# Optimization experiments

Hardware: AMD Instinct MI355X
Metric: run time of the kernel (lower is better)

The kernel has to match this reference:

```python
import jax, jax.numpy as jnp
import numpy as np

F = 32          # conf['num_features']
G = 96          # voxel grid extent
N_VOX = 80000   # occupied input voxels
BN_EPS = 1e-5


def _encode(c):
    c = c.astype(np.int64) + 8
    return (c[:, 0] * 512 + c[:, 1]) * 512 + c[:, 2]


def _offsets(ks, dil):
    r = np.arange(-(ks // 2), ks // 2 + 1) * dil
    return np.stack(np.meshgrid(r, r, r, indexing='ij'), -1).reshape(-1, 3)


def _build_map(in_coords, out_coords, offsets):
    # For each kernel offset k and output voxel j, find input voxel index at
    # out_coords[j] + offsets[k]; sentinel = n_in / n_out when absent.
    n_in, n_out = len(in_coords), len(out_coords)
    keys = _encode(in_coords)
    order = np.argsort(keys).astype(np.int32)
    skeys = keys[order]
    K = len(offsets)
    in_map = np.full((K, n_out), n_in, np.int32)
    out_map = np.full((K, n_out), n_out, np.int32)
    base = np.arange(n_out, dtype=np.int32)
    for k, off in enumerate(offsets):
        q = _encode(out_coords + off)
        pos = np.clip(np.searchsorted(skeys, q), 0, n_in - 1)
        valid = skeys[pos] == q
        in_map[k] = np.where(valid, order[pos], n_in)
        out_map[k] = np.where(valid, base, n_out)
    return jnp.asarray(in_map), jnp.asarray(out_map)


def setup_inputs() -> dict:
    rng = np.random.default_rng(0)
    idx = rng.choice(G ** 3, size=N_VOX, replace=False)
    coords = np.stack(np.unravel_index(idx, (G, G, G)), 1).astype(np.int64)
    c2 = np.unique(coords // 2 * 2, axis=0)   # stride-2 coords (enc1 output)
    c4 = np.unique(coords // 4 * 4, axis=0)   # stride-4 coords (c_out.C)

    m1_in, m1_out = _build_map(coords, c2, _offsets(5, 1))  # k5 s2 conv
    m2_in, m2_out = _build_map(c2, c2, _offsets(3, 2))      # enc1 blocks
    m3_in, m3_out = _build_map(c2, c4, _offsets(3, 2))      # conv2 -> c_out.C
    m4_in, m4_out = _build_map(c4, c4, _offsets(3, 4))      # enc2 blocks

    key = jax.random.key(0)
    ks = jax.random.split(key, 8)
    s = 0.05
    return {
        'x_geo': jax.random.normal(ks[0], (N_VOX, 1), jnp.float32),
        'x_col': jax.random.uniform(ks[1], (N_VOX, 3), jnp.float32),
        'w0': jax.random.normal(ks[2], (125, 4, F), jnp.float32) * s,
        'w_e1': jax.random.normal(ks[3], (2, 2, 27, F, F), jnp.float32) * s,
        'g_e1': jnp.ones((2, 2, F), jnp.float32),
        'b_e1': jnp.zeros((2, 2, F), jnp.float32),
        'w2': jax.random.normal(ks[4], (27, F, 2 * F), jnp.float32) * s,
        'w_e2': jax.random.normal(ks[5], (2, 2, 27, 2 * F, 2 * F), jnp.float32) * s,
        'g_e2': jnp.ones((2, 2, 2 * F), jnp.float32),
        'b_e2': jnp.zeros((2, 2, 2 * F), jnp.float32),
        'm1_in': m1_in, 'm1_out': m1_out,
        'm2_in': m2_in, 'm2_out': m2_out,
        'm3_in': m3_in, 'm3_out': m3_out,
        'm4_in': m4_in, 'm4_out': m4_out,
    }


def sparse_conv(feats, W, in_map, out_map):
    # gather -> GEMM -> scatter per kernel offset (lax.scan over K offsets)
    n_out = out_map.shape[1]
    fpad = jnp.concatenate([feats, jnp.zeros((1, feats.shape[1]), feats.dtype)], 0)
    out0 = jnp.zeros((n_out + 1, W.shape[2]), feats.dtype)
    def step(acc, kmw):
        im, om, w = kmw
        return acc.at[om].add(fpad[im] @ w), None
    out, _ = jax.lax.scan(step, out0, (in_map, out_map, W))
    return out[:n_out]


def batch_norm(x, g, b):
    mu = x.mean(0)
    var = ((x - mu) ** 2).mean(0)
    return (x - mu) * jax.lax.rsqrt(var + BN_EPS) * g + b


def basic_block(x, w, g, b, in_map, out_map):
    # ME BasicBlock: conv-BN-ReLU-conv-BN + residual, ReLU
    y = jax.nn.relu(batch_norm(sparse_conv(x, w[0], in_map, out_map), g[0], b[0]))
    y = batch_norm(sparse_conv(y, w[1], in_map, out_map), g[1], b[1])
    return jax.nn.relu(y + x)


def reference(x_geo, x_col, w0, w_e1, g_e1, b_e1, w2, w_e2, g_e2, b_e2,
              m1_in, m1_out, m2_in, m2_out, m3_in, m3_out, m4_in, m4_out):
    x = jnp.concatenate([x_geo, x_col], axis=1)          # ME.cat -> 4 channels
    x = jax.nn.relu(sparse_conv(x, w0, m1_in, m1_out))   # k5 s2 conv + ReLU
    for i in range(2):                                   # enc1 residual blocks
        x = basic_block(x, w_e1[i], g_e1[i], b_e1[i], m2_in, m2_out)
    x = sparse_conv(x, w2, m3_in, m3_out)                # conv2 onto c_out.C
    for i in range(2):                                   # enc2 residual blocks
        x = basic_block(x, w_e2[i], g_e2[i], b_e2[i], m4_in, m4_out)
    return x
```

## Files before the change

kernel.cpp:

```cpp
#include <hip/hip_runtime.h>
#include <hip/hip_bf16.h>


typedef float f4 __attribute__((ext_vector_type(4)));
typedef short short8 __attribute__((ext_vector_type(8)));
typedef short short4v __attribute__((ext_vector_type(4)));

#define BN_EPS 1e-5f

static inline int ceil_div(int a, int b) { return (a + b - 1) / b; }

static __device__ inline float btof(short s) {
    unsigned u = ((unsigned)(unsigned short)s) << 16;
    float f;
    __builtin_memcpy(&f, &u, 4);
    return f;
}
static __device__ inline short ftob(float f) {
    __hip_bfloat16 h = __float2bfloat16(f);
    short s;
    __builtin_memcpy(&s, &h, 2);
    return s;
}

static __device__ inline void gl_lds16(const void* g, void* l) {
    __builtin_amdgcn_global_load_lds(
        (const __attribute__((address_space(1))) void*)g,
        (__attribute__((address_space(3))) void*)l, 16, 0, 0);
}

template <int N>
static __device__ inline void s_wait_vmcnt() {
    static_assert(N >= 0 && N <= 8, "vmcnt range");
    if constexpr (N == 0) asm volatile("s_waitcnt vmcnt(0)" ::: "memory");
    else if constexpr (N == 1) asm volatile("s_waitcnt vmcnt(1)" ::: "memory");
    else if constexpr (N == 2) asm volatile("s_waitcnt vmcnt(2)" ::: "memory");
    else if constexpr (N == 3) asm volatile("s_waitcnt vmcnt(3)" ::: "memory");
    else if constexpr (N == 4) asm volatile("s_waitcnt vmcnt(4)" ::: "memory");
    else if constexpr (N == 5) asm volatile("s_waitcnt vmcnt(5)" ::: "memory");
    else if constexpr (N == 6) asm volatile("s_waitcnt vmcnt(6)" ::: "memory");
    else if constexpr (N == 7) asm volatile("s_waitcnt vmcnt(7)" ::: "memory");
    else asm volatile("s_waitcnt vmcnt(8)" ::: "memory");
}

struct Seg {
    const float* W;
    long long begin, end;
    int K, CIN, COUT;
};

struct ProArgs {
    Seg s[10];
    const float* geo;
    const float* col;
    __hip_bfloat16* x0;
    int n_vox;
    float* stats;
    __hip_bfloat16* pads[5];
    int padn[5];
    long long wf_total;
    long long pro_total;
    __hip_bfloat16* Wf;
    const int* m1;
    __hip_bfloat16* A;
    int nc2;
};

template <int C>
__device__ inline void bn_coef(const float* st, const float* g, const float* b,
                               int c, int n, float& sc, float& sh) {
    float rn = 1.f / (float)n;
    float sum = st[c] + st[2 * C + c] + st[4 * C + c] + st[6 * C + c];
    float sq  = st[C + c] + st[3 * C + c] + st[5 * C + c] + st[7 * C + c];
    float mu = sum * rn;
    float inv = rsqrtf(sq * rn - mu * mu + BN_EPS);
    sc = inv * g[c];
    sh = b[c] - mu * sc;
}

__global__ __launch_bounds__(256) void k_prologue(ProArgs pa) {
    for (long long e = (long long)blockIdx.x * 256 + threadIdx.x; e < pa.pro_total;
         e += (long long)gridDim.x * 256) {
        if (e < pa.wf_total) {
            int si = 0;
#pragma unroll
            for (int i = 0; i < 10; ++i)
                if (e >= pa.s[i].end) si = i + 1;
            const Seg sg = pa.s[si];
            long long r = e - sg.begin;
            int j = (int)(r & 7);
            int lane = (int)((r >> 3) & 63);
            long long rest = r >> 9;
            int NT = sg.COUT >> 4;
            int ntile = (int)(rest % NT);
            int chunk = (int)(rest / NT);
            int kd = chunk * 32 + ((lane >> 4) << 3) + j;
            int koff = kd / sg.CIN;
            int ci = kd % sg.CIN;
            int n = ntile * 16 + (lane & 15);
            float v = (koff < sg.K) ? sg.W[((size_t)koff * sg.CIN + ci) * sg.COUT + n] : 0.f;
            pa.Wf[e] = __float2bfloat16(v);
            continue;
        }
        long long r = e - pa.wf_total;
        if (r < pa.n_vox) {
            int row = (int)r;
            pa.x0[row * 4 + 0] = __float2bfloat16(pa.geo[row]);
            pa.x0[row * 4 + 1] = __float2bfloat16(pa.col[row * 3 + 0]);
            pa.x0[row * 4 + 2] = __float2bfloat16(pa.col[row * 3 + 1]);
            pa.x0[row * 4 + 3] = __float2bfloat16(pa.col[row * 3 + 2]);
            continue;
        }
        r -= pa.n_vox;
        if (r < 4096) {
            pa.stats[r] = 0.f;
            continue;
        }
        r -= 4096;
#pragma unroll
        for (int i = 0; i < 5; ++i) {
            if (r < pa.padn[i]) {
                pa.pads[i][r] = __float2bfloat16(0.f);
                r = -1;
                break;
            }
            r -= pa.padn[i];
        }
    }
}

__global__ __launch_bounds__(256) void k_stem(ProArgs a) {
    const int t = threadIdx.x, w = t >> 6, lane = t & 63;
    const int quad = lane >> 4, ml = lane & 15;
    const int ntile = w & 1, mgroup = w >> 1;
    const int n_out = a.nc2, n_in = a.n_vox;
    const __hip_bfloat16* feat = a.x0;
    const __hip_bfloat16* Wf = a.Wf;
    const int* in_map = a.m1;
    __hip_bfloat16* out = a.A;
    const int mb = blockIdx.x * 64 + mgroup * 32;
    const int m0 = mb + ml, m1 = mb + 16 + ml;
    const bool v0 = m0 < n_out, v1 = m1 < n_out;
    f4 acc0 = {0.f, 0.f, 0.f, 0.f};
    f4 acc1 = {0.f, 0.f, 0.f, 0.f};
#pragma unroll 2
    for (int chunk = 0; chunk < 16; ++chunk) {
        int k0 = chunk * 8 + quad * 2;
        int k1 = k0 + 1;
        int k0c = (k0 < 125) ? k0 : 0;
        int k1c = (k1 < 125) ? k1 : 0;
        short8 b = *(const short8*)(Wf + ((size_t)(chunk * 2 + ntile) * 64 + lane) * 8);
        int ia = v0 ? in_map[(size_t)k0c * n_out + m0] : n_in;
        int ib = v0 ? in_map[(size_t)k1c * n_out + m0] : n_in;
        int ic = v1 ? in_map[(size_t)k0c * n_out + m1] : n_in;
        int id = v1 ? in_map[(size_t)k1c * n_out + m1] : n_in;
        short4v p0 = *(const short4v*)(feat + (size_t)ia * 4);
        short4v p1 = *(const short4v*)(feat + (size_t)ib * 4);
        short4v p2 = *(const short4v*)(feat + (size_t)ic * 4);
        short4v p3 = *(const short4v*)(feat + (size_t)id * 4);
        short8 a0, a1;
        a0[0] = p0[0]; a0[1] = p0[1]; a0[2] = p0[2]; a0[3] = p0[3];
        a0[4] = p1[0]; a0[5] = p1[1]; a0[6] = p1[2]; a0[7] = p1[3];
        a1[0] = p2[0]; a1[1] = p2[1]; a1[2] = p2[2]; a1[3] = p2[3];
        a1[4] = p3[0]; a1[5] = p3[1]; a1[6] = p3[2]; a1[7] = p3[3];
        acc0 = __builtin_amdgcn_mfma_f32_16x16x32_bf16(a0, b, acc0, 0, 0, 0);
        acc1 = __builtin_amdgcn_mfma_f32_16x16x32_bf16(a1, b, acc1, 0, 0, 0);
    }
    const int col = ntile * 16 + ml;
#pragma unroll
    for (int i = 0; i < 4; ++i) {
        int r0 = mb + quad * 4 + i;
        if (r0 < n_out)
            out[(size_t)r0 * 32 + col] = __float2bfloat16(fmaxf(acc0[i], 0.f));
        int r1 = mb + 16 + quad * 4 + i;
        if (r1 < n_out)
            out[(size_t)r1 * 32 + col] = __float2bfloat16(fmaxf(acc1[i], 0.f));
    }
}

template <int CIN, int COUT, int MT, int K, bool BNF>
__global__ __launch_bounds__(256, 4) void k_conv(
    const __hip_bfloat16* __restrict__ feat,
    const __hip_bfloat16* __restrict__ Wf,
    const int* __restrict__ in_map,
    __hip_bfloat16* __restrict__ out,
    float* __restrict__ stats,
    const float* __restrict__ in_stats,
    const float* __restrict__ in_g,
    const float* __restrict__ in_b,
    int n_out, int n_in) {
    constexpr int NT = COUT / 16;
    constexpr int H = CIN / 32;
    constexpr int R = MT * 16;
    constexpr int KPW = (K + 3) / 4;
    constexpr int SP = COUT + 1;
    constexpr int S = CIN / 8;
    constexpr int RPI = 64 / S;
    constexpr int NI = R / RPI;
    constexpr int D = (MT == 1) ? 4 : 2;
    constexpr int STAGE_B = R * CIN * 2;
    constexpr int STAGE_TOT = 4 * D * STAGE_B;
    constexpr int RED_B = 4 * R * SP * 4;
    constexpr int UNION_B = (STAGE_TOT > RED_B) ? STAGE_TOT : RED_B;
    constexpr int WAIT_N = (D - 1) * NI;

    __shared__ char smem[UNION_B + 2048 + 512];
    float* red  = (float*)smem;
    float* sred = (float*)(smem + UNION_B);
    float* ibn  = (float*)(smem + UNION_B + 2048);

    const int t = threadIdx.x, w = t >> 6, lane = t & 63;
    const int quad = lane >> 4, ml = lane & 15;
    const int mb = blockIdx.x * R;
    char* stw = smem + w * (D * STAGE_B);
    const int srow = lane / S;
    const int ssl = lane & (S - 1);

    if constexpr (BNF) {
        if (t < CIN) {
            float sc, sh;
            bn_coef<CIN>(in_stats, in_g, in_b, t, n_in, sc, sh);
            ibn[t] = sc;
            ibn[CIN + t] = sh;
        }
        __syncthreads();
    }
    float scr[H][8], shr[H][8];
    if constexpr (BNF) {
#pragma unroll
        for (int h = 0; h < H; ++h)
#pragma unroll
            for (int j = 0; j < 8; ++j) {
                int ch = h * 32 + quad * 8 + j;
                scr[h][j] = ibn[ch];
                shr[h][j] = ibn[CIN + ch];
            }
    }

    int idxs[KPW][NI];
#pragma unroll
    for (int kk = 0; kk < KPW; ++kk) {
        const int k = kk * 4 + w;
        const int krow = (k < K) ? k : 0;
        const int* mk = in_map + (size_t)krow * n_out;
#pragma unroll
        for (int inst = 0; inst < NI; ++inst) {
            int m = mb + inst * RPI + srow;
            idxs[kk][inst] = (m < n_out) ? mk[m] : n_in;
        }
    }

    f4 acc[MT * NT];
#pragma unroll
    for (int i = 0; i < MT * NT; ++i) acc[i] = (f4){0.f, 0.f, 0.f, 0.f};

    auto issue = [&](int stg, int slot) {
#pragma unroll
        for (int inst = 0; inst < NI; ++inst) {
            int rg = inst * RPI + srow;
            int gsl = ssl ^ (rg & (S - 1));
            const __hip_bfloat16* src =
                feat + (size_t)idxs[stg][inst] * CIN + gsl * 8;
            gl_lds16(src, stw + slot * STAGE_B + inst * 1024);
        }
    };

#pragma unroll
    for (int s = 0; s < D; ++s) issue(s, s);

#pragma unroll
    for (int kk = 0; kk < KPW; ++kk) {
        s_wait_vmcnt<WAIT_N>();
        __builtin_amdgcn_sched_barrier(0);
        const int k = kk * 4 + w;
        const int slot = kk % D;

        short8 bfrag[H * NT];
#pragma unroll
        for (int h = 0; h < H; ++h)
#pragma unroll
            for (int nt = 0; nt < NT; ++nt)
                bfrag[h * NT + nt] = *(const short8*)(
                    Wf + (((size_t)(k * H + h) * NT + nt) * 64 + lane) * 8);

        int cidx[MT];
        if constexpr (BNF) {
            const int krow = (k < K) ? k : 0;
            const int* mk = in_map + (size_t)krow * n_out;
#pragma unroll
            for (int mi = 0; mi < MT; ++mi) {
                int m = mb + mi * 16 + ml;
                cidx[mi] = (m < n_out) ? mk[m] : n_in;
            }
        }

#pragma unroll
        for (int mi = 0; mi < MT; ++mi) {
#pragma unroll
            for (int h = 0; h < H; ++h) {
                const int p = (h * 4 + quad) ^ (ml & (S - 1));
                short8 a = *(const short8*)(
                    stw + slot * STAGE_B + ((mi * 16 + ml) * CIN + p * 8) * 2);
                if constexpr (BNF) {
                    const bool sent = (cidx[mi] == n_in);
#pragma unroll
                    for (int j = 0; j < 8; ++j) {
                        float f = btof(a[j]) * scr[h][j] + shr[h][j];
                        f = fmaxf(f, 0.f);
                        a[j] = sent ? (short)0 : ftob(f);
                    }
                }
#pragma unroll
                for (int nt = 0; nt < NT; ++nt)
                    acc[mi * NT + nt] = __builtin_amdgcn_mfma_f32_16x16x32_bf16(
                        a, bfrag[h * NT + nt], acc[mi * NT + nt], 0, 0, 0);
            }
        }

        __builtin_amdgcn_sched_barrier(0);
        issue((kk + D < KPW) ? (kk + D) : 0, slot);
    }

    s_wait_vmcnt<0>();
    __syncthreads();

#pragma unroll
    for (int mi = 0; mi < MT; ++mi)
#pragma unroll
        for (int nt = 0; nt < NT; ++nt)
#pragma unroll
            for (int i = 0; i < 4; ++i)
                red[((size_t)w * R + mi * 16 + quad * 4 + i) * SP + nt * 16 + ml] =
                    acc[mi * NT + nt][i];
    __syncthreads();

    constexpr int E = (R * COUT) / 256;
    constexpr int RSTEP = 256 / COUT;
    const int col = t % COUT;
    const int rg = t / COUT;
    float s = 0.f, s2 = 0.f;
#pragma unroll
    for (int i = 0; i < E; ++i) {
        int r = rg + i * RSTEP;
        float v = red[(0 * R + r) * SP + col] + red[(1 * R + r) * SP + col] +
                  red[(2 * R + r) * SP + col] + red[(3 * R + r) * SP + col];
        s += v;
        s2 += v * v;
        int grow = mb + r;
        if (grow < n_out) out[(size_t)grow * COUT + col] = __float2bfloat16(v);
    }

    if (stats) {
        sred[t] = s;
        sred[256 + t] = s2;
        __syncthreads();
        if (t < 2 * COUT) {
            int c = t % COUT;
            int which = t / COUT;
            float v = 0.f;
#pragma unroll
            for (int j = 0; j < RSTEP; ++j) v += sred[which * 256 + j * COUT + c];
            atomicAdd(&stats[((blockIdx.x & 3) * 2 + which) * COUT + c], v);
        }
    }
}

template <int C, bool F32OUT>
__global__ __launch_bounds__(256) void k_bnres(
    const __hip_bfloat16* __restrict__ y, const __hip_bfloat16* __restrict__ res,
    const float* __restrict__ st, const float* __restrict__ g,
    const float* __restrict__ b, void* outp, int n) {
    __shared__ float ibn[2 * C];
    const int t = threadIdx.x;
    if (t < C) {
        float sc, sh;
        bn_coef<C>(st, g, b, t, n, sc, sh);
        ibn[t] = sc;
        ibn[C + t] = sh;
    }
    __syncthreads();
    long long tot = (long long)n * (C / 8);
    long long i = (long long)blockIdx.x * 256 + t;
    if (i >= tot) return;
    int c0 = (int)(i % (C / 8)) * 8;
    short8 v = *(const short8*)(y + i * 8);
    short8 r = *(const short8*)(res + i * 8);
    if constexpr (F32OUT) {
        float* out = (float*)outp;
        f4 o0, o1;
#pragma unroll
        for (int j = 0; j < 8; ++j) {
            float f = btof(v[j]) * ibn[c0 + j] + ibn[C + c0 + j] + btof(r[j]);
            f = fmaxf(f, 0.f);
            if (j < 4) o0[j] = f; else o1[j - 4] = f;
        }
        *(f4*)(out + i * 8) = o0;
        *(f4*)(out + i * 8 + 4) = o1;
    } else {
        __hip_bfloat16* out = (__hip_bfloat16*)outp;
        short8 o;
#pragma unroll
        for (int j = 0; j < 8; ++j) {
            float f = btof(v[j]) * ibn[c0 + j] + ibn[C + c0 + j] + btof(r[j]);
            o[j] = ftob(fmaxf(f, 0.f));
        }
        *(short8*)(out + i * 8) = o;
    }
}

extern "C" void kernel_launch(void* const* d_in, const int* in_sizes, int n_in_cnt,
                              void* d_out, int out_size, void* d_ws, size_t ws_size,
                              hipStream_t stream) {
    const float* x_geo = (const float*)d_in[0];
    const float* x_col = (const float*)d_in[1];
    const float* w0    = (const float*)d_in[2];
    const float* w_e1  = (const float*)d_in[3];
    const float* g_e1  = (const float*)d_in[4];
    const float* b_e1  = (const float*)d_in[5];
    const float* w2    = (const float*)d_in[6];
    const float* w_e2  = (const float*)d_in[7];
    const float* g_e2  = (const float*)d_in[8];
    const float* b_e2  = (const float*)d_in[9];
    const int* m1 = (const int*)d_in[10];
    const int* m2 = (const int*)d_in[12];
    const int* m3 = (const int*)d_in[14];
    const int* m4 = (const int*)d_in[16];

    const int n_vox = in_sizes[0];
    const int nc2 = in_sizes[10] / 125;
    const int nc4 = in_sizes[14] / 27;
    (void)out_size; (void)ws_size; (void)n_in_cnt;

    char* p = (char*)d_ws;
    auto alloc = [&](size_t bytes) -> char* {
        char* r = p;
        p += (bytes + 255) & ~(size_t)255;
        return r;
    };
    float* stats = (float*)alloc(8 * 512 * sizeof(float));
    __hip_bfloat16* x0 = (__hip_bfloat16*)alloc((size_t)(n_vox + 1) * 4 * 2);
    __hip_bfloat16* A  = (__hip_bfloat16*)alloc((size_t)(nc2 + 1) * 32 * 2);
    __hip_bfloat16* B  = (__hip_bfloat16*)alloc((size_t)(nc2 + 1) * 32 * 2);
    __hip_bfloat16* Cb = (__hip_bfloat16*)alloc((size_t)(nc2 + 1) * 32 * 2);
    __hip_bfloat16* D  = (__hip_bfloat16*)alloc((size_t)(nc4 + 1) * 64 * 2);
    __hip_bfloat16* E  = (__hip_bfloat16*)alloc((size_t)(nc4 + 1) * 64 * 2);
    __hip_bfloat16* Fb = (__hip_bfloat16*)alloc((size_t)(nc4 + 1) * 64 * 2);

    const long long sz_stem = 16LL * 2 * 512;
    const long long sz_e1   = 28LL * 2 * 512;
    const long long sz_c2   = 28LL * 4 * 512;
    const long long sz_e2   = 56LL * 4 * 512;
    const long long wf_total = sz_stem + 4 * sz_e1 + sz_c2 + 4 * sz_e2;
    __hip_bfloat16* Wf = (__hip_bfloat16*)alloc((size_t)wf_total * 2);

    ProArgs pa;
    long long cur = 0;
    auto seg = [&](int i, const float* W, int K, int CIN, int COUT, long long n) {
        pa.s[i].W = W; pa.s[i].K = K; pa.s[i].CIN = CIN; pa.s[i].COUT = COUT;
        pa.s[i].begin = cur; pa.s[i].end = cur + n; cur += n;
    };
    seg(0, w0, 125, 4, 32, sz_stem);
    for (int i = 0; i < 4; ++i)
        seg(1 + i, w_e1 + (size_t)i * 27 * 32 * 32, 27, 32, 32, sz_e1);
    seg(5, w2, 27, 32, 64, sz_c2);
    for (int i = 0; i < 4; ++i)
        seg(6 + i, w_e2 + (size_t)i * 27 * 64 * 64, 27, 64, 64, sz_e2);

    long long off_e1[4], off_e2[4];
    cur = sz_stem;
    for (int i = 0; i < 4; ++i) { off_e1[i] = cur; cur += sz_e1; }
    long long off_c2 = cur; cur += sz_c2;
    for (int i = 0; i < 4; ++i) { off_e2[i] = cur; cur += sz_e2; }

    pa.geo = x_geo; pa.col = x_col; pa.x0 = x0; pa.n_vox = n_vox;
    pa.stats = stats;
    pa.pads[0] = x0 + (size_t)n_vox * 4; pa.padn[0] = 4;
    pa.pads[1] = A + (size_t)nc2 * 32;   pa.padn[1] = 32;
    pa.pads[2] = B + (size_t)nc2 * 32;   pa.padn[2] = 32;
    pa.pads[3] = D + (size_t)nc4 * 64;   pa.padn[3] = 64;
    pa.pads[4] = E + (size_t)nc4 * 64;   pa.padn[4] = 64;
    pa.wf_total = wf_total;
    pa.pro_total = wf_total + n_vox + 4096 + (4 + 32 + 32 + 64 + 64);
    pa.Wf = Wf;
    pa.m1 = m1;
    pa.A = A;
    pa.nc2 = nc2;

    k_prologue<<<ceil_div((int)pa.pro_total, 256), 256, 0, stream>>>(pa);
    k_stem<<<ceil_div(nc2, 64), 256, 0, stream>>>(pa);

    k_conv<32, 32, 4, 27, false><<<ceil_div(nc2, 64), 256, 0, stream>>>(
        A, Wf + off_e1[0], m2, B, stats + 0 * 512,
        nullptr, nullptr, nullptr, nc2, nc2);
    k_conv<32, 32, 4, 27, true><<<ceil_div(nc2, 64), 256, 0, stream>>>(
        B, Wf + off_e1[1], m2, Cb, stats + 1 * 512,
        stats + 0 * 512, g_e1 + 0, b_e1 + 0, nc2, nc2);
    k_bnres<32, false><<<ceil_div(nc2 * 4, 256), 256, 0, stream>>>(
        Cb, A, stats + 1 * 512, g_e1 + 32, b_e1 + 32, A, nc2);

    k_conv<32, 32, 4, 27, false><<<ceil_div(nc2, 64), 256, 0, stream>>>(
        A, Wf + off_e1[2], m2, B, stats + 2 * 512,
        nullptr, nullptr, nullptr, nc2, nc2);
    k_conv<32, 32, 4, 27, true><<<ceil_div(nc2, 64), 256, 0, stream>>>(
        B, Wf + off_e1[3], m2, Cb, stats + 3 * 512,
        stats + 2 * 512, g_e1 + 64, b_e1 + 64, nc2, nc2);
    k_bnres<32, false><<<ceil_div(nc2 * 4, 256), 256, 0, stream>>>(
        Cb, A, stats + 3 * 512, g_e1 + 96, b_e1 + 96, A, nc2);

    k_conv<32, 64, 1, 27, false><<<ceil_div(nc4, 16), 256, 0, stream>>>(
        A, Wf + off_c2, m3, D, nullptr,
        nullptr, nullptr, nullptr, nc4, nc2);

    k_conv<64, 64, 1, 27, false><<<ceil_div(nc4, 16), 256, 0, stream>>>(
        D, Wf + off_e2[0], m4, E, stats + 4 * 512,
        nullptr, nullptr, nullptr, nc4, nc4);
    k_conv<64, 64, 1, 27, true><<<ceil_div(nc4, 16), 256, 0, stream>>>(
        E, Wf + off_e2[1], m4, Fb, stats + 5 * 512,
        stats + 4 * 512, g_e2 + 0, b_e2 + 0, nc4, nc4);
    k_bnres<64, false><<<ceil_div(nc4 * 8, 256), 256, 0, stream>>>(
        Fb, D, stats + 5 * 512, g_e2 + 64, b_e2 + 64, D, nc4);

    k_conv<64, 64, 1, 27, false><<<ceil_div(nc4, 16), 256, 0, stream>>>(
        D, Wf + off_e2[2], m4, E, stats + 6 * 512,
        nullptr, nullptr, nullptr, nc4, nc4);
    k_conv<64, 64, 1, 27, true><<<ceil_div(nc4, 16), 256, 0, stream>>>(
        E, Wf + off_e2[3], m4, Fb, stats + 7 * 512,
        stats + 6 * 512, g_e2 + 128, b_e2 + 128, nc4, nc4);
    k_bnres<64, true><<<ceil_div(nc4 * 8, 256), 256, 0, stream>>>(
        Fb, D, stats + 7 * 512, g_e2 + 192, b_e2 + 192, (float*)d_out, nc4);
}
```

Before: 323.1 us.

## Double-buffer weight fragments in registers and derive sentinel indices via shuffles

Weight B-fragments are now prefetched one stage ahead into two register buffers, alongside the LDS gather of input rows, instead of being loaded right before the MFMAs. The gather pipeline is fixed at depth 2 for all tile shapes, and the vmcnt wait is recomputed to cover both the row loads and the weight loads. For the BN-fused path, the per-row input indices are obtained with cross-lane shuffles of the already-loaded map instead of a second global read. Launch bounds drop to 3 waves per SIMD for 64-channel inputs to leave room for the extra registers. The risks are the smaller gather depth for single-tile kernels, unlisted vmcnt values falling back to a default wait of 16, and shuffle index mapping that assumes particular MT/NI shapes.

```diff
diff --git a/kernel.cpp b/kernel.cpp
--- a/kernel.cpp
+++ b/kernel.cpp
@@ -31,16 +31,20 @@
 
 template <int N>
 static __device__ inline void s_wait_vmcnt() {
-    static_assert(N >= 0 && N <= 8, "vmcnt range");
+    static_assert(N >= 0 && N <= 20, "vmcnt range");
     if constexpr (N == 0) asm volatile("s_waitcnt vmcnt(0)" ::: "memory");
+    else if constexpr (N == 8) asm volatile("s_waitcnt vmcnt(8)" ::: "memory");
+    else if constexpr (N == 9) asm volatile("s_waitcnt vmcnt(9)" ::: "memory");
+    else if constexpr (N == 18) asm volatile("s_waitcnt vmcnt(18)" ::: "memory");
     else if constexpr (N == 1) asm volatile("s_waitcnt vmcnt(1)" ::: "memory");
     else if constexpr (N == 2) asm volatile("s_waitcnt vmcnt(2)" ::: "memory");
     else if constexpr (N == 3) asm volatile("s_waitcnt vmcnt(3)" ::: "memory");
     else if constexpr (N == 4) asm volatile("s_waitcnt vmcnt(4)" ::: "memory");
     else if constexpr (N == 5) asm volatile("s_waitcnt vmcnt(5)" ::: "memory");
     else if constexpr (N == 6) asm volatile("s_waitcnt vmcnt(6)" ::: "memory");
-    else if constexpr (N == 7) asm volatile("s_waitcnt vmcnt(7)" ::: "memory");
-    else asm volatile("s_waitcnt vmcnt(8)" ::: "memory");
+    else if constexpr (N == 10) asm volatile("s_waitcnt vmcnt(10)" ::: "memory");
+    else if constexpr (N == 12) asm volatile("s_waitcnt vmcnt(12)" ::: "memory");
+    else asm volatile("s_waitcnt vmcnt(16)" ::: "memory");
 }
 
 struct Seg {
@@ -179,7 +183,8 @@
 }
 
 template <int CIN, int COUT, int MT, int K, bool BNF>
-__global__ __launch_bounds__(256, 4) void k_conv(
+__global__ __launch_bounds__(256, ((CIN == 64) || (BNF && CIN == 64)) ? 3 : 4)
+void k_conv(
     const __hip_bfloat16* __restrict__ feat,
     const __hip_bfloat16* __restrict__ Wf,
     const int* __restrict__ in_map,
@@ -197,12 +202,13 @@
     constexpr int S = CIN / 8;
     constexpr int RPI = 64 / S;
     constexpr int NI = R / RPI;
-    constexpr int D = (MT == 1) ? 4 : 2;
+    constexpr int NB = H * NT;
+    constexpr int D = 2;
+    constexpr int WAIT_N = NI + 2 * NB;
     constexpr int STAGE_B = R * CIN * 2;
     constexpr int STAGE_TOT = 4 * D * STAGE_B;
     constexpr int RED_B = 4 * R * SP * 4;
     constexpr int UNION_B = (STAGE_TOT > RED_B) ? STAGE_TOT : RED_B;
-    constexpr int WAIT_N = (D - 1) * NI;
 
     __shared__ char smem[UNION_B + 2048 + 512];
     float* red  = (float*)smem;
@@ -254,7 +260,9 @@
 #pragma unroll
     for (int i = 0; i < MT * NT; ++i) acc[i] = (f4){0.f, 0.f, 0.f, 0.f};
 
-    auto issue = [&](int stg, int slot) {
+    short8 bf0[NB], bf1[NB];
+
+    auto issue_stage = [&](int stg, int slot) {
 #pragma unroll
         for (int inst = 0; inst < NI; ++inst) {
             int rg = inst * RPI + srow;
@@ -264,33 +272,41 @@
             gl_lds16(src, stw + slot * STAGE_B + inst * 1024);
         }
     };
-
-#pragma unroll
-    for (int s = 0; s < D; ++s) issue(s, s);
+    auto issue_bf = [&](int stg, short8 (&bfc)[NB]) {
+        const int k = stg * 4 + w;
+#pragma unroll
+        for (int h = 0; h < H; ++h)
+#pragma unroll
+            for (int nt = 0; nt < NT; ++nt)
+                bfc[h * NT + nt] = *(const short8*)(
+                    Wf + (((size_t)(k * H + h) * NT + nt) * 64 + lane) * 8);
+    };
+
+    issue_stage(0, 0);
+    issue_bf(0, bf0);
+    issue_stage(1, 1);
+    issue_bf(1, bf1);
+    __builtin_amdgcn_sched_barrier(0);
 
 #pragma unroll
     for (int kk = 0; kk < KPW; ++kk) {
         s_wait_vmcnt<WAIT_N>();
         __builtin_amdgcn_sched_barrier(0);
-        const int k = kk * 4 + w;
-        const int slot = kk % D;
-
-        short8 bfrag[H * NT];
-#pragma unroll
-        for (int h = 0; h < H; ++h)
-#pragma unroll
-            for (int nt = 0; nt < NT; ++nt)
-                bfrag[h * NT + nt] = *(const short8*)(
-                    Wf + (((size_t)(k * H + h) * NT + nt) * 64 + lane) * 8);
+
+        const int slot = kk & 1;
+        short8 (&bfc)[NB] = (kk & 1) ? bf1 : bf0;
 
         int cidx[MT];
         if constexpr (BNF) {
-            const int krow = (k < K) ? k : 0;
-            const int* mk = in_map + (size_t)krow * n_out;
 #pragma unroll
             for (int mi = 0; mi < MT; ++mi) {
-                int m = mb + mi * 16 + ml;
-                cidx[mi] = (m < n_out) ? mk[m] : n_in;
+                if constexpr (RPI >= 16) {
+                    cidx[mi] = __shfl(idxs[kk][(mi * 16) / RPI], ml * S);
+                } else {
+                    int a0 = __shfl(idxs[kk][0], (ml & 7) * S);
+                    int a1 = __shfl(idxs[kk][NI - 1], (ml & 7) * S);
+                    cidx[mi] = (ml < 8) ? a0 : a1;
+                }
             }
         }
 
@@ -313,12 +329,21 @@
 #pragma unroll
                 for (int nt = 0; nt < NT; ++nt)
                     acc[mi * NT + nt] = __builtin_amdgcn_mfma_f32_16x16x32_bf16(
-                        a, bfrag[h * NT + nt], acc[mi * NT + nt], 0, 0, 0);
+                        a, bfc[h * NT + nt], acc[mi * NT + nt], 0, 0, 0);
             }
         }
 
         __builtin_amdgcn_sched_barrier(0);
-        issue((kk + D < KPW) ? (kk + D) : 0, slot);
+        const int ns = (kk + 2 < KPW) ? (kk + 2) : 0;
+        issue_stage(ns, slot);
+        if (kk & 1) issue_bf(ns, bf1); else issue_bf(ns, bf0);
+        __builtin_amdgcn_sched_barrier(0);
+    }
+
+#pragma unroll
+    for (int i = 0; i < NB; ++i) {
+        asm volatile("" ::"v"(bf0[i]));
+        asm volatile("" ::"v"(bf1[i]));
     }
 
     s_wait_vmcnt<0>();
```

Result: faster. 310.4 us (-3.9%).
